# Optimization experiments

Hardware: AMD Instinct MI355X
Metric: run time of the kernel (lower is better)

## Reference

```python
import jax, jax.numpy as jnp
import numpy as np

TINY = 1e-6
MIN_DEG, MAX_DEG = 0, 16

# 3x21 icosahedral basis used for the background (non-diag) IPE
P = jnp.asarray(np.array([
    0.8506508, 0.0, 0.5257311, 0.809017, 0.5, 0.309017, 0.5257311, 0.8506508, 0.0,
    1.0, 0.0, 0.0, 0.809017, 0.5, -0.309017, 0.8506508, 0.0, -0.5257311, 0.309017,
    0.809017, -0.5, 0.0, 0.5257311, -0.8506508, 0.5, 0.309017, -0.809017, 0.0, 1.0,
    0.0, -0.5257311, 0.8506508, 0.0, -0.309017, 0.809017, -0.5, 0.0, 0.5257311,
    0.8506508, -0.309017, 0.809017, 0.5, 0.309017, 0.809017, 0.5, 0.5, 0.309017,
    0.809017, 0.5, -0.309017, 0.809017, 0.0, 0.0, 1.0, -0.5, 0.309017, 0.809017,
    -0.809017, 0.5, 0.309017, -0.809017, 0.5, -0.309017], dtype=np.float32).reshape(3, 21))


def setup_inputs() -> dict:
    key = jax.random.key(0)
    k1, k2, k3, k4, k5 = jax.random.split(key, 5)
    N, Ns = 2048, 64
    ray_o = jax.random.normal(k1, (N, 3), dtype=jnp.float32)
    ray_d = jax.random.normal(k2, (N, 3), dtype=jnp.float32)
    fg_z_vals = jnp.sort(jax.random.uniform(k3, (N, Ns + 1), minval=0.1, maxval=5.0), axis=-1)
    bg_z_vals = jnp.sort(jax.random.uniform(k4, (N, Ns + 1), minval=1.0, maxval=50.0), axis=-1)
    radii = jax.random.uniform(k5, (N, 1), minval=0.005, maxval=0.02)
    return {"ray_o": ray_o, "ray_d": ray_d, "fg_z_vals": fg_z_vals,
            "bg_z_vals": bg_z_vals, "radii": radii}


def _frustum_moments(t0, t1, base_radius):
    mu = (t0 + t1) / 2.0
    hw = (t1 - t0) / 2.0
    denom = 3.0 * mu ** 2 + hw ** 2
    t_mean = mu + 2.0 * mu * hw ** 2 / denom
    t_var = hw ** 2 / 3.0 - (4.0 / 15.0) * (hw ** 4 * (12.0 * mu ** 2 - hw ** 2) / denom ** 2)
    r_var = base_radius ** 2 * (mu ** 2 / 4.0 + (5.0 / 12.0) * hw ** 2 - (4.0 / 15.0) * hw ** 4 / denom)
    return t_mean, t_var, r_var


def cast_rays_diag(t_vals, origins, directions, radii):
    t_mean, t_var, r_var = _frustum_moments(t_vals[..., :-1], t_vals[..., 1:], radii)
    d = directions[..., None, :]                      # [N,1,3]
    mean = d * t_mean[..., None]                      # [N,Ns,3]
    d_mag_sq = jnp.maximum(1e-8, jnp.sum(d ** 2, axis=-1, keepdims=True))
    d_outer_diag = d ** 2
    null_outer_diag = 1.0 - d_outer_diag / d_mag_sq
    cov_diag = t_var[..., None] * d_outer_diag + r_var[..., None] * null_outer_diag
    return mean + origins[..., None, :], cov_diag


def cast_rays_full(t_vals, origins, directions, radii):
    t_mean, t_var, r_var = _frustum_moments(t_vals[..., :-1], t_vals[..., 1:], radii)
    d = directions[..., None, :]                      # [N,1,3]
    mean = d * t_mean[..., None]                      # [N,Ns,3]
    d_mag_sq = jnp.maximum(1e-8, jnp.sum(d ** 2, axis=-1, keepdims=True))
    d_outer = d[..., :, None] * d[..., None, :]       # [N,1,3,3]
    eye = jnp.eye(3, dtype=d.dtype)
    null_outer = eye - d[..., :, None] * (d / d_mag_sq)[..., None, :]
    cov = t_var[..., None, None] * d_outer + r_var[..., None, None] * null_outer
    return mean + origins[..., None, :], cov          # [N,Ns,3], [N,Ns,3,3]


def _contract_point(x):
    n = jnp.linalg.norm(x) + TINY
    return (2.0 - 1.0 / n) * (x / n)


def contract_gaussian(mean, cov_full):
    N, Ns = mean.shape[0], mean.shape[1]
    flat = mean.reshape(-1, 3)
    J = jax.vmap(jax.jacfwd(_contract_point))(flat).reshape(N, Ns, 3, 3)
    n = jnp.linalg.norm(mean, axis=-1, keepdims=True) + TINY
    mean_c = (2.0 - 1.0 / n) * (mean / n)
    cov_c = jnp.einsum('nsij,nsjk,nslk->nsil', J, cov_full, J)
    return mean_c, cov_c


def expected_sin(x, x_var):
    return jnp.exp(-0.5 * x_var) * jnp.sin(x)


def ipe_diag(x, x_cov_diag, min_deg, max_deg):
    scales = 2.0 ** jnp.arange(min_deg, max_deg, dtype=x.dtype)   # [L]
    N, Ns = x.shape[0], x.shape[1]
    y = (x[..., None, :] * scales[:, None]).reshape(N, Ns, -1)                 # [N,Ns,L*3]
    y_var = (x_cov_diag[..., None, :] * (scales ** 2)[:, None]).reshape(N, Ns, -1)
    return expected_sin(jnp.concatenate([y, y + 0.5 * jnp.pi], axis=-1),
                        jnp.concatenate([y_var, y_var], axis=-1))


def ipe_full(x, x_cov, min_deg, max_deg):
    y = jnp.matmul(x, P)                                                        # [N,Ns,21]
    y_var = jnp.einsum('nsab,bk,ak->nsk', x_cov, P, P)                          # [N,Ns,21]
    scales = 2.0 ** jnp.arange(min_deg, max_deg, dtype=x.dtype)
    N, Ns = x.shape[0], x.shape[1]
    y = (y[..., None, :] * scales[:, None]).reshape(N, Ns, -1)                  # [N,Ns,L*21]
    y_var = (y_var[..., None, :] * (scales ** 2)[:, None]).reshape(N, Ns, -1)
    return expected_sin(jnp.concatenate([y, y + 0.5 * jnp.pi], axis=-1),
                        jnp.concatenate([y_var, y_var], axis=-1))


def reference(ray_o, ray_d, fg_z_vals, bg_z_vals, radii):
    # foreground: diagonal-cov cone cast + diagonal IPE  -> [N,Ns,96]
    fg_mean, fg_cov_diag = cast_rays_diag(fg_z_vals, ray_o, ray_d, radii)
    enc_fg = ipe_diag(fg_mean, fg_cov_diag, MIN_DEG, MAX_DEG)
    # background: full-cov cone cast + contraction Jacobian + basis IPE -> [N,Ns,672]
    bg_mean, bg_cov = cast_rays_full(bg_z_vals, ray_o, ray_d, radii)
    mean_c, cov_c = contract_gaussian(bg_mean, bg_cov)
    enc_bg = ipe_full(mean_c, cov_c, MIN_DEG, MAX_DEG)
    return jnp.concatenate([enc_fg, enc_bg], axis=-1)                            # [N,Ns,768]
```

## Files before the change

kernel.cpp:

```cpp
#include <hip/hip_runtime.h>
#include <math.h>

#define NS 64
#define INV2PI  0.15915494309189535f
#define NEGHL2E (-0.72134752044448170f)

__constant__ float c_P[63] = {
  0.8506508f, 0.0f, 0.5257311f, 0.809017f, 0.5f, 0.309017f, 0.5257311f,
  0.8506508f, 0.0f, 1.0f, 0.0f, 0.0f, 0.809017f, 0.5f, -0.309017f,
  0.8506508f, 0.0f, -0.5257311f, 0.309017f, 0.809017f, -0.5f,
  0.0f, 0.5257311f, -0.8506508f, 0.5f, 0.309017f, -0.809017f, 0.0f, 1.0f,
  0.0f, -0.5257311f, 0.8506508f, 0.0f, -0.309017f, 0.809017f, -0.5f, 0.0f,
  0.5257311f, 0.8506508f, -0.309017f, 0.809017f, 0.5f,
  0.309017f, 0.809017f, 0.5f, 0.5f, 0.309017f, 0.809017f, 0.5f, -0.309017f,
  0.809017f, 0.0f, 0.0f, 1.0f, -0.5f, 0.309017f, 0.809017f, -0.809017f,
  0.5f, 0.309017f, -0.809017f, 0.5f, -0.309017f
};

struct Moments { float t_mean, t_var, r_var; };

__device__ inline Moments frustum_moments(float t0, float t1, float radius) {
    float mu  = 0.5f * (t0 + t1);
    float hw  = 0.5f * (t1 - t0);
    float mu2 = mu * mu, hw2 = hw * hw;
    float denom = 3.0f * mu2 + hw2;
    float inv_d = 1.0f / denom;
    float hw4 = hw2 * hw2;
    Moments m;
    m.t_mean = mu + 2.0f * mu * hw2 * inv_d;
    m.t_var  = hw2 * (1.0f / 3.0f)
             - (4.0f / 15.0f) * (hw4 * (12.0f * mu2 - hw2) * inv_d * inv_d);
    m.r_var  = radius * radius *
               (0.25f * mu2 + (5.0f / 12.0f) * hw2 - (4.0f / 15.0f) * hw4 * inv_d);
    return m;
}

__global__ __launch_bounds__(256) void mipnerf_enc(
    const float* __restrict__ ray_o,
    const float* __restrict__ ray_d,
    const float* __restrict__ fgz,
    const float* __restrict__ bgz,
    const float* __restrict__ radii,
    float* __restrict__ out)
{
    const int n   = blockIdx.x;
    const int tid = threadIdx.x;

    __shared__ float sXV[NS * 50];
    __shared__ float sCore[NS * 11];

    const float ox = ray_o[3 * n + 0], oy = ray_o[3 * n + 1], oz = ray_o[3 * n + 2];
    const float dx = ray_d[3 * n + 0], dy = ray_d[3 * n + 1], dz = ray_d[3 * n + 2];
    const float rad = radii[n];
    const float dm = fmaxf(1e-8f, dx * dx + dy * dy + dz * dz);
    const float inv_dm = 1.0f / dm;

    if (tid < NS) {
        const int s = tid;
        {
            float t0 = fgz[(NS + 1) * n + s];
            float t1 = fgz[(NS + 1) * n + s + 1];
            Moments mm = frustum_moments(t0, t1, rad);
            float d3[3] = {dx, dy, dz};
            float o3[3] = {ox, oy, oz};
            #pragma unroll
            for (int i = 0; i < 3; ++i) {
                float m  = o3[i] + d3[i] * mm.t_mean;
                float dd = d3[i] * d3[i];
                float cd = mm.t_var * dd + mm.r_var * (1.0f - dd * inv_dm);
                sXV[s * 50 + 2 * (21 + i) + 0] = m  * INV2PI;
                sXV[s * 50 + 2 * (21 + i) + 1] = cd * NEGHL2E;
            }
        }
        {
            float t0 = bgz[(NS + 1) * n + s];
            float t1 = bgz[(NS + 1) * n + s + 1];
            Moments mm = frustum_moments(t0, t1, rad);
            float x0 = ox + dx * mm.t_mean;
            float x1 = oy + dy * mm.t_mean;
            float x2 = oz + dz * mm.t_mean;
            float a  = mm.t_var - mm.r_var * inv_dm;
            float rv = mm.r_var;
            float rn2 = x0 * x0 + x1 * x1 + x2 * x2;
            float rn  = sqrtf(rn2);
            float nn  = rn + 1e-6f;
            float inn = 1.0f / nn;
            float g   = (2.0f * nn - 1.0f) * inn * inn;
            float gp  = 2.0f * (1.0f - nn) * inn * inn * inn;
            float h   = gp / rn;
            float xd  = x0 * dx + x1 * dy + x2 * dz;
            float hxd = h * xd;
            float u0 = g * dx + hxd * x0;
            float u1 = g * dy + hxd * x1;
            float u2 = g * dz + hxd * x2;
            float w  = 2.0f * g * h + h * h * rn2;
            float* cr = &sCore[s * 11];
            cr[0] = x0; cr[1] = x1; cr[2] = x2;
            cr[3] = u0; cr[4] = u1; cr[5] = u2;
            cr[6] = g;  cr[7] = a;  cr[8] = rv * g * g; cr[9] = rv * w;
        }
    }
    __syncthreads();

    #pragma unroll
    for (int j = 0; j < 6; ++j) {
        int i = tid + 256 * j;
        if (i < 21 * NS) {
            int k = i >> 6;
            int s = i & (NS - 1);
            const float p0 = c_P[k], p1 = c_P[21 + k], p2 = c_P[42 + k];
            const float* cr = &sCore[s * 11];
            float x0 = cr[0], x1 = cr[1], x2 = cr[2];
            float u0 = cr[3], u1 = cr[4], u2 = cr[5];
            float g = cr[6], c1 = cr[7], c2 = cr[8], c3 = cr[9];
            float dpx = p0 * x0 + p1 * x1 + p2 * x2;
            float dpu = p0 * u0 + p1 * u1 + p2 * u2;
            float pp  = p0 * p0 + p1 * p1 + p2 * p2;
            float y   = g * dpx;
            float yv  = c1 * dpu * dpu + c2 * pp + c3 * dpx * dpx;
            sXV[s * 50 + 2 * k + 0] = y  * INV2PI;
            sXV[s * 50 + 2 * k + 1] = yv * NEGHL2E;
        }
    }
    __syncthreads();

    float4* __restrict__ outv = reinterpret_cast<float4*>(out) + (size_t)n * (NS * 768 / 4);
    for (int it = 0; it < 48; ++it) {
        int idx = tid + 256 * it;
        int s   = idx / 192;
        int c   = (idx - s * 192) * 4;
        int deg, src, srcLo, srcHi;
        float phq;
        if (c < 96) {
            int ph = (c >= 48) ? 1 : 0;
            int jj = c - 48 * ph;
            deg = jj / 3;
            src = 21 + (jj - 3 * deg);
            srcLo = 21; srcHi = 24;
            phq = 0.25f * (float)ph;
        } else {
            int local = c - 96;
            int ph = (local >= 336) ? 1 : 0;
            int jj = local - 336 * ph;
            deg = jj / 21;
            src = jj - 21 * deg;
            srcLo = 0; srcHi = 21;
            phq = 0.25f * (float)ph;
        }
        const float* rowXV = &sXV[s * 50];
        float vals[4];
        #pragma unroll
        for (int q = 0; q < 4; ++q) {
            float X = rowXV[2 * src + 0];
            float V = rowXV[2 * src + 1];
            float sf  = __int_as_float((127 + deg) << 23);
            float s2f = __int_as_float((127 + 2 * deg) << 23);
            float e = __builtin_amdgcn_exp2f(V * s2f);
            float r = __builtin_amdgcn_fractf(X * sf + phq);
            vals[q] = e * __builtin_amdgcn_sinf(r);
            if (++src == srcHi) { src = srcLo; ++deg; }
        }
        outv[idx] = make_float4(vals[0], vals[1], vals[2], vals[3]);
    }
}

extern "C" void kernel_launch(void* const* d_in, const int* in_sizes, int n_in,
                              void* d_out, int out_size, void* d_ws, size_t ws_size,
                              hipStream_t stream) {
    const float* ray_o = (const float*)d_in[0];
    const float* ray_d = (const float*)d_in[1];
    const float* fgz   = (const float*)d_in[2];
    const float* bgz   = (const float*)d_in[3];
    const float* radii = (const float*)d_in[4];
    float* out = (float*)d_out;
    const int N = in_sizes[0] / 3;
    mipnerf_enc<<<N, 256, 0, stream>>>(ray_o, ray_d, fgz, bgz, radii, out);
}
```

Before: 414.6 us.

## Compute each coordinate's degree sweep per thread, sharing exp across sin phases

The output stage is remapped so that each thread owns one (sample, coordinate) pair and loops over all 16 degrees. It computes the exp2 attenuation once and reuses it for both the sin and the cos (phase-shifted) outputs. It also reads X/V once as a float2 and drops the per-element index decoding and division. This cuts transcendental and index arithmetic. In exchange the coalesced float4 stores become strided scalar stores, which may lower write efficiency.

```diff
diff --git a/kernel.cpp b/kernel.cpp
--- a/kernel.cpp
+++ b/kernel.cpp
@@ -124,43 +124,31 @@
     }
     __syncthreads();
 
-    float4* __restrict__ outv = reinterpret_cast<float4*>(out) + (size_t)n * (NS * 768 / 4);
-    for (int it = 0; it < 48; ++it) {
-        int idx = tid + 256 * it;
-        int s   = idx / 192;
-        int c   = (idx - s * 192) * 4;
-        int deg, src, srcLo, srcHi;
-        float phq;
-        if (c < 96) {
-            int ph = (c >= 48) ? 1 : 0;
-            int jj = c - 48 * ph;
-            deg = jj / 3;
-            src = 21 + (jj - 3 * deg);
-            srcLo = 21; srcHi = 24;
-            phq = 0.25f * (float)ph;
-        } else {
-            int local = c - 96;
-            int ph = (local >= 336) ? 1 : 0;
-            int jj = local - 336 * ph;
-            deg = jj / 21;
-            src = jj - 21 * deg;
-            srcLo = 0; srcHi = 21;
-            phq = 0.25f * (float)ph;
+    float* __restrict__ op = out + (size_t)n * (NS * 768);
+    #pragma unroll
+    for (int it = 0; it < 6; ++it) {
+        int w = tid + 256 * it;
+        int s = (int)((unsigned)w / 24u);
+        int j = w - 24 * s;
+        const float2 xv = *(const float2*)&sXV[s * 50 + 2 * j];
+        const float X = xv.x, V = xv.y;
+        const bool bg = (j < 21);
+        int off0 = s * 768 + (bg ? (96 + j) : (j - 21));
+        int off1 = off0 + (bg ? 336 : 48);
+        const int dstr = bg ? 21 : 3;
+        #pragma unroll
+        for (int d = 0; d < 16; ++d) {
+            const float sf  = (float)(1 << d);
+            const float s2f = sf * sf;
+            float xs = X * sf;
+            float e  = __builtin_amdgcn_exp2f(V * s2f);
+            float r0 = __builtin_amdgcn_fractf(xs);
+            float r1 = __builtin_amdgcn_fractf(xs + 0.25f);
+            op[off0] = e * __builtin_amdgcn_sinf(r0);
+            op[off1] = e * __builtin_amdgcn_sinf(r1);
+            off0 += dstr;
+            off1 += dstr;
         }
-        const float* rowXV = &sXV[s * 50];
-        float vals[4];
-        #pragma unroll
-        for (int q = 0; q < 4; ++q) {
-            float X = rowXV[2 * src + 0];
-            float V = rowXV[2 * src + 1];
-            float sf  = __int_as_float((127 + deg) << 23);
-            float s2f = __int_as_float((127 + 2 * deg) << 23);
-            float e = __builtin_amdgcn_exp2f(V * s2f);
-            float r = __builtin_amdgcn_fractf(X * sf + phq);
-            vals[q] = e * __builtin_amdgcn_sinf(r);
-            if (++src == srcHi) { src = srcLo; ++deg; }
-        }
-        outv[idx] = make_float4(vals[0], vals[1], vals[2], vals[3]);
     }
 }
 
```

Result: slower. 433.1 us (+4.5%).
